# Kernel tuning notes

Hardware: AMD Instinct MI355X
Metric: run time of the kernel (lower is better)

The kernel has to match this reference:

```python
import jax, jax.numpy as jnp
import numpy as np

N_CLUSTERS = 512
TEMPERATURE = 0.1


def setup_inputs() -> dict:
    key = jax.random.key(0)
    k1, k2 = jax.random.split(key)
    x = jax.random.normal(k1, (32, 1024, 256), dtype=jnp.float32)
    centroids = jax.random.normal(k2, (N_CLUSTERS, 256), dtype=jnp.float32)
    return {"x": x, "centroids": centroids}


def reference(x, centroids):
    # Flatten non-cluster axes into a sample axis: [N, D]
    B, S, D = x.shape
    xf = x.reshape(-1, D)  # [N, D]
    x_sq = jnp.sum(xf * xf, axis=-1, keepdims=True)           # [N, 1]
    c_sq = jnp.sum(centroids * centroids, axis=-1)             # [K]
    cross = jnp.einsum('nd,kd->nk', xf, centroids)             # [N, K]
    dists = x_sq - 2.0 * cross + c_sq[None, :]                 # [N, K]
    # Temperature-scaled soft assignments
    assignments = jax.nn.softmax(-dists / TEMPERATURE, axis=-1)  # [N, K]
    # Restore leading (non-feature) dims, append cluster axis
    return assignments.reshape(B, S, N_CLUSTERS)
```

## Files before the change

kernel.cpp:

```cpp
#include <hip/hip_runtime.h>

#define NROWS 32768
#define KC 512
#define DDIM 256
#define BM 128
#define BK 32
#define KCH (DDIM / BK)
#define CHUNK_USH (KC * BK)

typedef __attribute__((ext_vector_type(8))) short bf16x8;
typedef __attribute__((ext_vector_type(4))) float f32x4;

union U8 { unsigned short u[8]; bf16x8 v; };

__device__ __forceinline__ unsigned short f2bf(float f) {
    union { float f; unsigned int u; } a; a.f = f;
    unsigned int r = a.u + 0x7fffu + ((a.u >> 16) & 1u);
    return (unsigned short)(r >> 16);
}
__device__ __forceinline__ float bf2f(unsigned short h) {
    union { unsigned int u; float f; } a; a.u = ((unsigned int)h) << 16;
    return a.f;
}
__device__ __forceinline__ void ld16(const void* g, void* l) {
    __builtin_amdgcn_global_load_lds(
        (const __attribute__((address_space(1))) unsigned int*)g,
        (__attribute__((address_space(3))) unsigned int*)l, 16, 0, 0);
}

__global__ __launch_bounds__(64) void prep_c(const float* __restrict__ c,
                                             unsigned short* __restrict__ bhi,
                                             unsigned short* __restrict__ blo,
                                             float* __restrict__ csq10) {
    const int n = blockIdx.x, lane = threadIdx.x;
    const int d0 = lane * 4;
    float4 v = ((const float4*)(c + (size_t)n * DDIM))[lane];
    float vv[4] = {v.x, v.y, v.z, v.w};
    unsigned short hh[4], ll[4];
    float ssq = 0.f;
    #pragma unroll
    for (int i = 0; i < 4; ++i) {
        ssq += vv[i] * vv[i];
        hh[i] = f2bf(vv[i]);
        ll[i] = f2bf(vv[i] - bf2f(hh[i]));
    }
    #pragma unroll
    for (int off = 32; off; off >>= 1) ssq += __shfl_xor(ssq, off);
    if (lane == 0) csq10[n] = 10.f * ssq;
    const int ks = d0 >> 5;
    const int q  = (d0 >> 3) & 3;
    const int s  = q ^ ((n >> 1) & 3);
    const size_t dst = (size_t)ks * CHUNK_USH + (n * 4 + s) * 8 + (d0 & 7);
    *(ushort4*)(bhi + dst) = make_ushort4(hh[0], hh[1], hh[2], hh[3]);
    *(ushort4*)(blo + dst) = make_ushort4(ll[0], ll[1], ll[2], ll[3]);
}

union SmemU {
    struct { unsigned short Bh[2][CHUNK_USH], Bl[2][CHUNK_USH]; } k;
    float lbuf[32 * 516];
};

__global__ __launch_bounds__(512, 2) void kmeans_mfma(
    const float* __restrict__ x, const unsigned short* __restrict__ bhi,
    const unsigned short* __restrict__ blo, const float* __restrict__ csq10,
    float* __restrict__ out) {
    __shared__ __align__(16) SmemU sm;
    __shared__ float red[2][2][BM];

    const int tid  = threadIdx.x;
    const int w    = tid >> 6, lane = tid & 63;
    const int wm   = w >> 1, wn = w & 1;
    const int cc   = lane & 15, q = lane >> 4;
    const int row0 = blockIdx.x * BM;

    f32x4 acc[2][16];
    #pragma unroll
    for (int mt = 0; mt < 2; ++mt)
        #pragma unroll
        for (int t = 0; t < 16; ++t) acc[mt][t] = (f32x4){0.f, 0.f, 0.f, 0.f};

    const float* xA0 = x + (size_t)(row0 + wm * 32 + cc) * DDIM + q * 8;
    const float* xA1 = xA0 + (size_t)16 * DDIM;
    const int sF = q ^ ((cc >> 1) & 3);
    const int bF = (4 * cc + sF) * 8;
    const int dmaOff = (w * 4) * 512;

    #pragma unroll
    for (int j = 0; j < 4; ++j) {
        const int o = dmaOff + j * 512;
        ld16(bhi + o + lane * 8, &sm.k.Bh[0][o]);
        ld16(blo + o + lane * 8, &sm.k.Bl[0][o]);
    }
    float4 c00 = *(const float4*)xA0;
    float4 c01 = *(const float4*)(xA0 + 4);
    float4 c10 = *(const float4*)xA1;
    float4 c11 = *(const float4*)(xA1 + 4);
    __syncthreads();

    for (int ks = 0; ks < KCH; ++ks) {
        const int pp = ks & 1;
        float4 n00, n01, n10, n11;
        if (ks < KCH - 1) {
            const size_t cb = (size_t)(ks + 1) * CHUNK_USH;
            #pragma unroll
            for (int j = 0; j < 4; ++j) {
                const int o = dmaOff + j * 512;
                ld16(bhi + cb + o + lane * 8, &sm.k.Bh[1 - pp][o]);
                ld16(blo + cb + o + lane * 8, &sm.k.Bl[1 - pp][o]);
            }
            const int kn = (ks + 1) * BK;
            n00 = *(const float4*)(xA0 + kn);
            n01 = *(const float4*)(xA0 + kn + 4);
            n10 = *(const float4*)(xA1 + kn);
            n11 = *(const float4*)(xA1 + kn + 4);
        }
        bf16x8 ah[2], al[2];
        {
            float v0[8] = {c00.x, c00.y, c00.z, c00.w, c01.x, c01.y, c01.z, c01.w};
            float v1[8] = {c10.x, c10.y, c10.z, c10.w, c11.x, c11.y, c11.z, c11.w};
            U8 H0, L0, H1, L1;
            #pragma unroll
            for (int i = 0; i < 8; ++i) {
                H0.u[i] = f2bf(v0[i]); L0.u[i] = f2bf(v0[i] - bf2f(H0.u[i]));
                H1.u[i] = f2bf(v1[i]); L1.u[i] = f2bf(v1[i] - bf2f(H1.u[i]));
            }
            ah[0] = H0.v; al[0] = L0.v; ah[1] = H1.v; al[1] = L1.v;
        }
        #pragma unroll
        for (int t = 0; t < 16; ++t) {
            const int bo = (wn * 16 + t) * 512 + bF;
            bf16x8 bh = *(const bf16x8*)&sm.k.Bh[pp][bo];
            bf16x8 bl = *(const bf16x8*)&sm.k.Bl[pp][bo];
            acc[0][t] = __builtin_amdgcn_mfma_f32_16x16x32_bf16(ah[0], bh, acc[0][t], 0, 0, 0);
            acc[1][t] = __builtin_amdgcn_mfma_f32_16x16x32_bf16(ah[1], bh, acc[1][t], 0, 0, 0);
            acc[0][t] = __builtin_amdgcn_mfma_f32_16x16x32_bf16(ah[0], bl, acc[0][t], 0, 0, 0);
            acc[1][t] = __builtin_amdgcn_mfma_f32_16x16x32_bf16(ah[1], bl, acc[1][t], 0, 0, 0);
            acc[0][t] = __builtin_amdgcn_mfma_f32_16x16x32_bf16(al[0], bh, acc[0][t], 0, 0, 0);
            acc[1][t] = __builtin_amdgcn_mfma_f32_16x16x32_bf16(al[1], bh, acc[1][t], 0, 0, 0);
        }
        c00 = n00; c01 = n01; c10 = n10; c11 = n11;
        __syncthreads();
    }

    float csqv[16];
    #pragma unroll
    for (int t = 0; t < 16; ++t) csqv[t] = csq10[wn * 256 + t * 16 + cc];
    const int rb = wm * 32 + q * 4;
    float M[2][4], I[2][4];
    #pragma unroll
    for (int mt = 0; mt < 2; ++mt)
        #pragma unroll
        for (int g = 0; g < 4; ++g) {
            float pm = -1e30f;
            #pragma unroll
            for (int t = 0; t < 16; ++t) pm = fmaxf(pm, 20.f * acc[mt][t][g] - csqv[t]);
            #pragma unroll
            for (int off = 1; off < 16; off <<= 1) pm = fmaxf(pm, __shfl_xor(pm, off));
            if (cc == 0) red[0][wn][rb + mt * 16 + g] = pm;
            M[mt][g] = pm;
        }
    __syncthreads();
    #pragma unroll
    for (int mt = 0; mt < 2; ++mt)
        #pragma unroll
        for (int g = 0; g < 4; ++g) {
            M[mt][g] = fmaxf(M[mt][g], red[0][1 - wn][rb + mt * 16 + g]);
            float ps = 0.f;
            #pragma unroll
            for (int t = 0; t < 16; ++t) ps += __expf(20.f * acc[mt][t][g] - csqv[t] - M[mt][g]);
            #pragma unroll
            for (int off = 1; off < 16; off <<= 1) ps += __shfl_xor(ps, off);
            if (cc == 0) red[1][wn][rb + mt * 16 + g] = ps;
        }
    __syncthreads();
    #pragma unroll
    for (int mt = 0; mt < 2; ++mt)
        #pragma unroll
        for (int g = 0; g < 4; ++g)
            I[mt][g] = 1.f / (red[1][0][rb + mt * 16 + g] + red[1][1][rb + mt * 16 + g]);

    #pragma unroll
    for (int p = 0; p < 4; ++p) {
        if (wm == p) {
            #pragma unroll
            for (int mt = 0; mt < 2; ++mt)
                #pragma unroll
                for (int g = 0; g < 4; ++g) {
                    const int   lr = mt * 16 + q * 4 + g;
                    const float mg = M[mt][g], ig = I[mt][g];
                    #pragma unroll
                    for (int t = 0; t < 16; ++t)
                        sm.lbuf[lr * 516 + wn * 256 + t * 16 + cc] =
                            __expf(20.f * acc[mt][t][g] - csqv[t] - mg) * ig;
                }
        }
        __syncthreads();
        #pragma unroll
        for (int j = 0; j < 8; ++j) {
            const int f    = j * 512 + tid;
            const int lrow = f >> 7;
            const int c4   = f & 127;
            float4    v    = *(const float4*)&sm.lbuf[lrow * 516 + c4 * 4];
            *(float4*)(out + (size_t)(row0 + p * 32 + lrow) * KC + c4 * 4) = v;
        }
        __syncthreads();
    }
}

extern "C" void kernel_launch(void* const* d_in, const int* in_sizes, int n_in,
                              void* d_out, int out_size, void* d_ws, size_t ws_size,
                              hipStream_t stream) {
    const float* x   = (const float*)d_in[0];
    const float* c   = (const float*)d_in[1];
    float*       out = (float*)d_out;

    unsigned short* bhi   = (unsigned short*)d_ws;
    unsigned short* blo   = bhi + (size_t)KCH * CHUNK_USH;
    float*          csq10 = (float*)(blo + (size_t)KCH * CHUNK_USH);

    prep_c<<<KC, 64, 0, stream>>>(c, bhi, blo, csq10);
    kmeans_mfma<<<NROWS / BM, 512, 0, stream>>>(x, bhi, blo, csq10, out);
}
```

Baseline: 118.6 us.

## Switch to 32x32x16 MFMA with smaller row tiles and 256-thread blocks

Replaces the 16x16x32 bf16 MFMA tiling with 32x32x16 MFMA instructions. Each wave now covers 32 rows by 256 clusters using 8 accumulator tiles. Block size drops to 64 rows and 256 threads, and the K chunk shrinks to 16, which halves the shared-memory B buffers and doubles the number of K iterations. The centroid prep layout and LDS swizzle are reworked to match the new operand layout, and the softmax reductions now precompute max and inverse sum into a shared table. The aim is to lower LDS traffic per FLOP and raise occupancy, at the cost of more barriers per row.

```diff
diff --git a/kernel.cpp b/kernel.cpp
--- a/kernel.cpp
+++ b/kernel.cpp
@@ -3,13 +3,13 @@
 #define NROWS 32768
 #define KC 512
 #define DDIM 256
-#define BM 128
-#define BK 32
+#define BM 64
+#define BK 16
 #define KCH (DDIM / BK)
 #define CHUNK_USH (KC * BK)
 
-typedef __attribute__((ext_vector_type(8))) short bf16x8;
-typedef __attribute__((ext_vector_type(4))) float f32x4;
+typedef __attribute__((ext_vector_type(8)))  short bf16x8;
+typedef __attribute__((ext_vector_type(16))) float f32x16;
 
 union U8 { unsigned short u[8]; bf16x8 v; };
 
@@ -47,42 +47,43 @@
     #pragma unroll
     for (int off = 32; off; off >>= 1) ssq += __shfl_xor(ssq, off);
     if (lane == 0) csq10[n] = 10.f * ssq;
-    const int ks = d0 >> 5;
-    const int q  = (d0 >> 3) & 3;
-    const int s  = q ^ ((n >> 1) & 3);
-    const size_t dst = (size_t)ks * CHUNK_USH + (n * 4 + s) * 8 + (d0 & 7);
+    const int ks = d0 >> 4;
+    const int h  = (d0 >> 3) & 1;
+    const int j0 = d0 & 7;
+    const int c5 = n & 31, tile = n >> 5;
+    const int p  = (2 * c5 + h) ^ ((c5 >> 2) & 1);
+    const size_t dst = (size_t)ks * CHUNK_USH + tile * 512 + p * 8 + j0;
     *(ushort4*)(bhi + dst) = make_ushort4(hh[0], hh[1], hh[2], hh[3]);
     *(ushort4*)(blo + dst) = make_ushort4(ll[0], ll[1], ll[2], ll[3]);
 }
 
 union SmemU {
     struct { unsigned short Bh[2][CHUNK_USH], Bl[2][CHUNK_USH]; } k;
-    float lbuf[32 * 516];
+    float lbuf[16 * 516];
 };
 
-__global__ __launch_bounds__(512, 2) void kmeans_mfma(
+__global__ __launch_bounds__(256, 2) void kmeans_mfma(
     const float* __restrict__ x, const unsigned short* __restrict__ bhi,
     const unsigned short* __restrict__ blo, const float* __restrict__ csq10,
     float* __restrict__ out) {
     __shared__ __align__(16) SmemU sm;
-    __shared__ float red[2][2][BM];
+    __shared__ float  red0[2][BM], red1[2][BM];
+    __shared__ float2 MI[BM];
 
     const int tid  = threadIdx.x;
     const int w    = tid >> 6, lane = tid & 63;
     const int wm   = w >> 1, wn = w & 1;
-    const int cc   = lane & 15, q = lane >> 4;
+    const int c5   = lane & 31, h = lane >> 5;
     const int row0 = blockIdx.x * BM;
 
-    f32x4 acc[2][16];
-    #pragma unroll
-    for (int mt = 0; mt < 2; ++mt)
-        #pragma unroll
-        for (int t = 0; t < 16; ++t) acc[mt][t] = (f32x4){0.f, 0.f, 0.f, 0.f};
-
-    const float* xA0 = x + (size_t)(row0 + wm * 32 + cc) * DDIM + q * 8;
-    const float* xA1 = xA0 + (size_t)16 * DDIM;
-    const int sF = q ^ ((cc >> 1) & 3);
-    const int bF = (4 * cc + sF) * 8;
+    f32x16 acc[8];
+    #pragma unroll
+    for (int t = 0; t < 8; ++t)
+        #pragma unroll
+        for (int r = 0; r < 16; ++r) acc[t][r] = 0.f;
+
+    const float* xrow = x + (size_t)(row0 + wm * 32 + c5) * DDIM + h * 8;
+    const int bRd    = ((2 * c5 + h) ^ ((c5 >> 2) & 1)) * 8;
     const int dmaOff = (w * 4) * 512;
 
     #pragma unroll
@@ -91,15 +92,13 @@
         ld16(bhi + o + lane * 8, &sm.k.Bh[0][o]);
         ld16(blo + o + lane * 8, &sm.k.Bl[0][o]);
     }
-    float4 c00 = *(const float4*)xA0;
-    float4 c01 = *(const float4*)(xA0 + 4);
-    float4 c10 = *(const float4*)xA1;
-    float4 c11 = *(const float4*)(xA1 + 4);
+    float4 a0 = *(const float4*)xrow;
+    float4 a1 = *(const float4*)(xrow + 4);
     __syncthreads();
 
     for (int ks = 0; ks < KCH; ++ks) {
         const int pp = ks & 1;
-        float4 n00, n01, n10, n11;
+        float4 n0, n1;
         if (ks < KCH - 1) {
             const size_t cb = (size_t)(ks + 1) * CHUNK_USH;
             #pragma unroll
@@ -108,100 +107,88 @@
                 ld16(bhi + cb + o + lane * 8, &sm.k.Bh[1 - pp][o]);
                 ld16(blo + cb + o + lane * 8, &sm.k.Bl[1 - pp][o]);
             }
-            const int kn = (ks + 1) * BK;
-            n00 = *(const float4*)(xA0 + kn);
-            n01 = *(const float4*)(xA0 + kn + 4);
-            n10 = *(const float4*)(xA1 + kn);
-            n11 = *(const float4*)(xA1 + kn + 4);
-        }
-        bf16x8 ah[2], al[2];
+            n0 = *(const float4*)(xrow + (ks + 1) * BK);
+            n1 = *(const float4*)(xrow + (ks + 1) * BK + 4);
+        }
+        bf16x8 ah, al;
         {
-            float v0[8] = {c00.x, c00.y, c00.z, c00.w, c01.x, c01.y, c01.z, c01.w};
-            float v1[8] = {c10.x, c10.y, c10.z, c10.w, c11.x, c11.y, c11.z, c11.w};
-            U8 H0, L0, H1, L1;
+            float v8[8] = {a0.x, a0.y, a0.z, a0.w, a1.x, a1.y, a1.z, a1.w};
+            U8 H, L;
             #pragma unroll
             for (int i = 0; i < 8; ++i) {
-                H0.u[i] = f2bf(v0[i]); L0.u[i] = f2bf(v0[i] - bf2f(H0.u[i]));
-                H1.u[i] = f2bf(v1[i]); L1.u[i] = f2bf(v1[i] - bf2f(H1.u[i]));
+                H.u[i] = f2bf(v8[i]);
+                L.u[i] = f2bf(v8[i] - bf2f(H.u[i]));
             }
-            ah[0] = H0.v; al[0] = L0.v; ah[1] = H1.v; al[1] = L1.v;
-        }
-        #pragma unroll
-        for (int t = 0; t < 16; ++t) {
-            const int bo = (wn * 16 + t) * 512 + bF;
+            ah = H.v; al = L.v;
+        }
+        #pragma unroll
+        for (int t = 0; t < 8; ++t) {
+            const int bo = (wn * 8 + t) * 512 + bRd;
             bf16x8 bh = *(const bf16x8*)&sm.k.Bh[pp][bo];
             bf16x8 bl = *(const bf16x8*)&sm.k.Bl[pp][bo];
-            acc[0][t] = __builtin_amdgcn_mfma_f32_16x16x32_bf16(ah[0], bh, acc[0][t], 0, 0, 0);
-            acc[1][t] = __builtin_amdgcn_mfma_f32_16x16x32_bf16(ah[1], bh, acc[1][t], 0, 0, 0);
-            acc[0][t] = __builtin_amdgcn_mfma_f32_16x16x32_bf16(ah[0], bl, acc[0][t], 0, 0, 0);
-            acc[1][t] = __builtin_amdgcn_mfma_f32_16x16x32_bf16(ah[1], bl, acc[1][t], 0, 0, 0);
-            acc[0][t] = __builtin_amdgcn_mfma_f32_16x16x32_bf16(al[0], bh, acc[0][t], 0, 0, 0);
-            acc[1][t] = __builtin_amdgcn_mfma_f32_16x16x32_bf16(al[1], bh, acc[1][t], 0, 0, 0);
-        }
-        c00 = n00; c01 = n01; c10 = n10; c11 = n11;
+            acc[t] = __builtin_amdgcn_mfma_f32_32x32x16_bf16(ah, bh, acc[t], 0, 0, 0);
+            acc[t] = __builtin_amdgcn_mfma_f32_32x32x16_bf16(ah, bl, acc[t], 0, 0, 0);
+            acc[t] = __builtin_amdgcn_mfma_f32_32x32x16_bf16(al, bh, acc[t], 0, 0, 0);
+        }
+        a0 = n0; a1 = n1;
         __syncthreads();
     }
 
-    float csqv[16];
-    #pragma unroll
-    for (int t = 0; t < 16; ++t) csqv[t] = csq10[wn * 256 + t * 16 + cc];
-    const int rb = wm * 32 + q * 4;
-    float M[2][4], I[2][4];
-    #pragma unroll
-    for (int mt = 0; mt < 2; ++mt)
-        #pragma unroll
-        for (int g = 0; g < 4; ++g) {
-            float pm = -1e30f;
+    float csqv[8];
+    #pragma unroll
+    for (int t = 0; t < 8; ++t) csqv[t] = csq10[wn * 256 + t * 32 + c5];
+
+    #pragma unroll
+    for (int r = 0; r < 16; ++r) {
+        float pm = -1e30f;
+        #pragma unroll
+        for (int t = 0; t < 8; ++t) pm = fmaxf(pm, 20.f * acc[t][r] - csqv[t]);
+        #pragma unroll
+        for (int off = 1; off < 32; off <<= 1) pm = fmaxf(pm, __shfl_xor(pm, off));
+        if (c5 == 0) red0[wn][wm * 32 + (r & 3) + 8 * (r >> 2) + 4 * h] = pm;
+    }
+    __syncthreads();
+    #pragma unroll
+    for (int r = 0; r < 16; ++r) {
+        const int row = wm * 32 + (r & 3) + 8 * (r >> 2) + 4 * h;
+        const float Mf = fmaxf(red0[0][row], red0[1][row]);
+        float ps = 0.f;
+        #pragma unroll
+        for (int t = 0; t < 8; ++t) ps += __expf(20.f * acc[t][r] - csqv[t] - Mf);
+        #pragma unroll
+        for (int off = 1; off < 32; off <<= 1) ps += __shfl_xor(ps, off);
+        if (c5 == 0) red1[wn][row] = ps;
+    }
+    __syncthreads();
+    if (tid < BM) {
+        const float Mf = fmaxf(red0[0][tid], red0[1][tid]);
+        const float Sf = red1[0][tid] + red1[1][tid];
+        MI[tid] = make_float2(Mf, 1.f / Sf);
+    }
+    __syncthreads();
+
+    #pragma unroll
+    for (int p = 0; p < 4; ++p) {
+        if (wm == (p >> 1)) {
             #pragma unroll
-            for (int t = 0; t < 16; ++t) pm = fmaxf(pm, 20.f * acc[mt][t][g] - csqv[t]);
-            #pragma unroll
-            for (int off = 1; off < 16; off <<= 1) pm = fmaxf(pm, __shfl_xor(pm, off));
-            if (cc == 0) red[0][wn][rb + mt * 16 + g] = pm;
-            M[mt][g] = pm;
-        }
-    __syncthreads();
-    #pragma unroll
-    for (int mt = 0; mt < 2; ++mt)
-        #pragma unroll
-        for (int g = 0; g < 4; ++g) {
-            M[mt][g] = fmaxf(M[mt][g], red[0][1 - wn][rb + mt * 16 + g]);
-            float ps = 0.f;
-            #pragma unroll
-            for (int t = 0; t < 16; ++t) ps += __expf(20.f * acc[mt][t][g] - csqv[t] - M[mt][g]);
-            #pragma unroll
-            for (int off = 1; off < 16; off <<= 1) ps += __shfl_xor(ps, off);
-            if (cc == 0) red[1][wn][rb + mt * 16 + g] = ps;
-        }
-    __syncthreads();
-    #pragma unroll
-    for (int mt = 0; mt < 2; ++mt)
-        #pragma unroll
-        for (int g = 0; g < 4; ++g)
-            I[mt][g] = 1.f / (red[1][0][rb + mt * 16 + g] + red[1][1][rb + mt * 16 + g]);
-
-    #pragma unroll
-    for (int p = 0; p < 4; ++p) {
-        if (wm == p) {
-            #pragma unroll
-            for (int mt = 0; mt < 2; ++mt)
+            for (int i = 0; i < 8; ++i) {
+                const int    rr  = (p & 1) * 8 + i;
+                const int    lr  = (i & 3) + 8 * (i >> 2) + 4 * h;
+                const float2 mi  = MI[p * 16 + lr];
                 #pragma unroll
-                for (int g = 0; g < 4; ++g) {
-                    const int   lr = mt * 16 + q * 4 + g;
-                    const float mg = M[mt][g], ig = I[mt][g];
-                    #pragma unroll
-                    for (int t = 0; t < 16; ++t)
-                        sm.lbuf[lr * 516 + wn * 256 + t * 16 + cc] =
-                            __expf(20.f * acc[mt][t][g] - csqv[t] - mg) * ig;
-                }
+                for (int t = 0; t < 8; ++t)
+                    sm.lbuf[lr * 516 + wn * 256 + t * 32 + c5] =
+                        __expf(20.f * acc[t][rr] - csqv[t] - mi.x) * mi.y;
+            }
         }
         __syncthreads();
         #pragma unroll
         for (int j = 0; j < 8; ++j) {
-            const int f    = j * 512 + tid;
+            const int f    = j * 256 + tid;
             const int lrow = f >> 7;
             const int c4   = f & 127;
             float4    v    = *(const float4*)&sm.lbuf[lrow * 516 + c4 * 4];
-            *(float4*)(out + (size_t)(row0 + p * 32 + lrow) * KC + c4 * 4) = v;
+            *(float4*)(out + (size_t)(row0 + p * 16 + lrow) * KC + c4 * 4) = v;
         }
         __syncthreads();
     }
@@ -219,5 +206,5 @@
     float*          csq10 = (float*)(blo + (size_t)KCH * CHUNK_USH);
 
     prep_c<<<KC, 64, 0, stream>>>(c, bhi, blo, csq10);
-    kmeans_mfma<<<NROWS / BM, 512, 0, stream>>>(x, bhi, blo, csq10, out);
-}
+    kmeans_mfma<<<NROWS / BM, 256, 0, stream>>>(x, bhi, blo, csq10, out);
+}
```

After: 123.0 us. 1.04x slower.

## Reshape warp tiling to 2x4 with 64-row by 128-cluster tiles per warp

Applied to the files above, without the earlier changes.

Changes the warp layout from 4x2 (32 rows by 256 clusters per warp) to 2x4 (64 rows by 128 clusters per warp). Each warp now converts four A fragments and reads eight B fragments from LDS per k-chunk instead of two and sixteen. This cuts LDS B traffic per MFMA and raises reuse of each B load across four M tiles. It also makes the softmax reduction four-way across warps, adding an MI shared array and an extra barrier, and raises register pressure for the A fragments.

```diff
diff --git a/kernel.cpp b/kernel.cpp
--- a/kernel.cpp
+++ b/kernel.cpp
@@ -65,22 +65,25 @@
     const unsigned short* __restrict__ blo, const float* __restrict__ csq10,
     float* __restrict__ out) {
     __shared__ __align__(16) SmemU sm;
-    __shared__ float red[2][2][BM];
+    __shared__ float  red0[4][BM], red1[4][BM];
+    __shared__ float2 MI[BM];
 
     const int tid  = threadIdx.x;
     const int w    = tid >> 6, lane = tid & 63;
-    const int wm   = w >> 1, wn = w & 1;
+    const int wm   = w >> 2, wn = w & 3;
     const int cc   = lane & 15, q = lane >> 4;
     const int row0 = blockIdx.x * BM;
 
-    f32x4 acc[2][16];
-    #pragma unroll
-    for (int mt = 0; mt < 2; ++mt)
-        #pragma unroll
-        for (int t = 0; t < 16; ++t) acc[mt][t] = (f32x4){0.f, 0.f, 0.f, 0.f};
-
-    const float* xA0 = x + (size_t)(row0 + wm * 32 + cc) * DDIM + q * 8;
-    const float* xA1 = xA0 + (size_t)16 * DDIM;
+    f32x4 acc[4][8];
+    #pragma unroll
+    for (int mt = 0; mt < 4; ++mt)
+        #pragma unroll
+        for (int t = 0; t < 8; ++t) acc[mt][t] = (f32x4){0.f, 0.f, 0.f, 0.f};
+
+    const float* xA[4];
+    #pragma unroll
+    for (int mt = 0; mt < 4; ++mt)
+        xA[mt] = x + (size_t)(row0 + wm * 64 + mt * 16 + cc) * DDIM + q * 8;
     const int sF = q ^ ((cc >> 1) & 3);
     const int bF = (4 * cc + sF) * 8;
     const int dmaOff = (w * 4) * 512;
@@ -91,15 +94,17 @@
         ld16(bhi + o + lane * 8, &sm.k.Bh[0][o]);
         ld16(blo + o + lane * 8, &sm.k.Bl[0][o]);
     }
-    float4 c00 = *(const float4*)xA0;
-    float4 c01 = *(const float4*)(xA0 + 4);
-    float4 c10 = *(const float4*)xA1;
-    float4 c11 = *(const float4*)(xA1 + 4);
+    float4 a[4][2];
+    #pragma unroll
+    for (int mt = 0; mt < 4; ++mt) {
+        a[mt][0] = *(const float4*)(xA[mt]);
+        a[mt][1] = *(const float4*)(xA[mt] + 4);
+    }
     __syncthreads();
 
     for (int ks = 0; ks < KCH; ++ks) {
         const int pp = ks & 1;
-        float4 n00, n01, n10, n11;
+        float4 n[4][2];
         if (ks < KCH - 1) {
             const size_t cb = (size_t)(ks + 1) * CHUNK_USH;
             #pragma unroll
@@ -109,90 +114,99 @@
                 ld16(blo + cb + o + lane * 8, &sm.k.Bl[1 - pp][o]);
             }
             const int kn = (ks + 1) * BK;
-            n00 = *(const float4*)(xA0 + kn);
-            n01 = *(const float4*)(xA0 + kn + 4);
-            n10 = *(const float4*)(xA1 + kn);
-            n11 = *(const float4*)(xA1 + kn + 4);
-        }
-        bf16x8 ah[2], al[2];
-        {
-            float v0[8] = {c00.x, c00.y, c00.z, c00.w, c01.x, c01.y, c01.z, c01.w};
-            float v1[8] = {c10.x, c10.y, c10.z, c10.w, c11.x, c11.y, c11.z, c11.w};
-            U8 H0, L0, H1, L1;
+            #pragma unroll
+            for (int mt = 0; mt < 4; ++mt) {
+                n[mt][0] = *(const float4*)(xA[mt] + kn);
+                n[mt][1] = *(const float4*)(xA[mt] + kn + 4);
+            }
+        }
+        bf16x8 ah[4], al[4];
+        #pragma unroll
+        for (int mt = 0; mt < 4; ++mt) {
+            float v8[8] = {a[mt][0].x, a[mt][0].y, a[mt][0].z, a[mt][0].w,
+                           a[mt][1].x, a[mt][1].y, a[mt][1].z, a[mt][1].w};
+            U8 H, L;
             #pragma unroll
             for (int i = 0; i < 8; ++i) {
-                H0.u[i] = f2bf(v0[i]); L0.u[i] = f2bf(v0[i] - bf2f(H0.u[i]));
-                H1.u[i] = f2bf(v1[i]); L1.u[i] = f2bf(v1[i] - bf2f(H1.u[i]));
-            }
-            ah[0] = H0.v; al[0] = L0.v; ah[1] = H1.v; al[1] = L1.v;
-        }
-        #pragma unroll
-        for (int t = 0; t < 16; ++t) {
-            const int bo = (wn * 16 + t) * 512 + bF;
+                H.u[i] = f2bf(v8[i]);
+                L.u[i] = f2bf(v8[i] - bf2f(H.u[i]));
+            }
+            ah[mt] = H.v; al[mt] = L.v;
+        }
+        #pragma unroll
+        for (int t = 0; t < 8; ++t) {
+            const int bo = (wn * 8 + t) * 512 + bF;
             bf16x8 bh = *(const bf16x8*)&sm.k.Bh[pp][bo];
             bf16x8 bl = *(const bf16x8*)&sm.k.Bl[pp][bo];
-            acc[0][t] = __builtin_amdgcn_mfma_f32_16x16x32_bf16(ah[0], bh, acc[0][t], 0, 0, 0);
-            acc[1][t] = __builtin_amdgcn_mfma_f32_16x16x32_bf16(ah[1], bh, acc[1][t], 0, 0, 0);
-            acc[0][t] = __builtin_amdgcn_mfma_f32_16x16x32_bf16(ah[0], bl, acc[0][t], 0, 0, 0);
-            acc[1][t] = __builtin_amdgcn_mfma_f32_16x16x32_bf16(ah[1], bl, acc[1][t], 0, 0, 0);
-            acc[0][t] = __builtin_amdgcn_mfma_f32_16x16x32_bf16(al[0], bh, acc[0][t], 0, 0, 0);
-            acc[1][t] = __builtin_amdgcn_mfma_f32_16x16x32_bf16(al[1], bh, acc[1][t], 0, 0, 0);
-        }
-        c00 = n00; c01 = n01; c10 = n10; c11 = n11;
+            #pragma unroll
+            for (int mt = 0; mt < 4; ++mt) {
+                acc[mt][t] = __builtin_amdgcn_mfma_f32_16x16x32_bf16(ah[mt], bh, acc[mt][t], 0, 0, 0);
+                acc[mt][t] = __builtin_amdgcn_mfma_f32_16x16x32_bf16(ah[mt], bl, acc[mt][t], 0, 0, 0);
+                acc[mt][t] = __builtin_amdgcn_mfma_f32_16x16x32_bf16(al[mt], bh, acc[mt][t], 0, 0, 0);
+            }
+        }
+        #pragma unroll
+        for (int mt = 0; mt < 4; ++mt) { a[mt][0] = n[mt][0]; a[mt][1] = n[mt][1]; }
         __syncthreads();
     }
 
-    float csqv[16];
-    #pragma unroll
-    for (int t = 0; t < 16; ++t) csqv[t] = csq10[wn * 256 + t * 16 + cc];
-    const int rb = wm * 32 + q * 4;
-    float M[2][4], I[2][4];
-    #pragma unroll
-    for (int mt = 0; mt < 2; ++mt)
+    float csqv[8];
+    #pragma unroll
+    for (int t = 0; t < 8; ++t) csqv[t] = csq10[wn * 128 + t * 16 + cc];
+
+    #pragma unroll
+    for (int mt = 0; mt < 4; ++mt)
         #pragma unroll
         for (int g = 0; g < 4; ++g) {
             float pm = -1e30f;
             #pragma unroll
-            for (int t = 0; t < 16; ++t) pm = fmaxf(pm, 20.f * acc[mt][t][g] - csqv[t]);
+            for (int t = 0; t < 8; ++t) pm = fmaxf(pm, 20.f * acc[mt][t][g] - csqv[t]);
             #pragma unroll
             for (int off = 1; off < 16; off <<= 1) pm = fmaxf(pm, __shfl_xor(pm, off));
-            if (cc == 0) red[0][wn][rb + mt * 16 + g] = pm;
-            M[mt][g] = pm;
-        }
-    __syncthreads();
-    #pragma unroll
-    for (int mt = 0; mt < 2; ++mt)
+            if (cc == 0) red0[wn][wm * 64 + mt * 16 + q * 4 + g] = pm;
+        }
+    __syncthreads();
+    float M[4][4];
+    #pragma unroll
+    for (int mt = 0; mt < 4; ++mt)
         #pragma unroll
         for (int g = 0; g < 4; ++g) {
-            M[mt][g] = fmaxf(M[mt][g], red[0][1 - wn][rb + mt * 16 + g]);
+            const int row = wm * 64 + mt * 16 + q * 4 + g;
+            float Mf = fmaxf(fmaxf(red0[0][row], red0[1][row]),
+                             fmaxf(red0[2][row], red0[3][row]));
+            M[mt][g] = Mf;
             float ps = 0.f;
             #pragma unroll
-            for (int t = 0; t < 16; ++t) ps += __expf(20.f * acc[mt][t][g] - csqv[t] - M[mt][g]);
+            for (int t = 0; t < 8; ++t) ps += __expf(20.f * acc[mt][t][g] - csqv[t] - Mf);
             #pragma unroll
             for (int off = 1; off < 16; off <<= 1) ps += __shfl_xor(ps, off);
-            if (cc == 0) red[1][wn][rb + mt * 16 + g] = ps;
-        }
-    __syncthreads();
-    #pragma unroll
-    for (int mt = 0; mt < 2; ++mt)
-        #pragma unroll
-        for (int g = 0; g < 4; ++g)
-            I[mt][g] = 1.f / (red[1][0][rb + mt * 16 + g] + red[1][1][rb + mt * 16 + g]);
+            if (cc == 0) red1[wn][row] = ps;
+        }
+    __syncthreads();
+    if (tid < BM) {
+        const float Mf = fmaxf(fmaxf(red0[0][tid], red0[1][tid]),
+                               fmaxf(red0[2][tid], red0[3][tid]));
+        const float Sf = red1[0][tid] + red1[1][tid] + red1[2][tid] + red1[3][tid];
+        MI[tid] = make_float2(Mf, 1.f / Sf);
+    }
+    __syncthreads();
 
     #pragma unroll
     for (int p = 0; p < 4; ++p) {
-        if (wm == p) {
-            #pragma unroll
-            for (int mt = 0; mt < 2; ++mt)
+        if (wm == (p >> 1)) {
+            #pragma unroll
+            for (int mi = 0; mi < 2; ++mi) {
+                const int mt = (p & 1) * 2 + mi;
                 #pragma unroll
                 for (int g = 0; g < 4; ++g) {
-                    const int   lr = mt * 16 + q * 4 + g;
-                    const float mg = M[mt][g], ig = I[mt][g];
+                    const int    lr  = mi * 16 + q * 4 + g;
+                    const float2 mi2 = MI[p * 32 + lr];
                     #pragma unroll
-                    for (int t = 0; t < 16; ++t)
-                        sm.lbuf[lr * 516 + wn * 256 + t * 16 + cc] =
-                            __expf(20.f * acc[mt][t][g] - csqv[t] - mg) * ig;
+                    for (int t = 0; t < 8; ++t)
+                        sm.lbuf[lr * 516 + wn * 128 + t * 16 + cc] =
+                            __expf(20.f * acc[mt][t][g] - csqv[t] - mi2.x) * mi2.y;
                 }
+            }
         }
         __syncthreads();
         #pragma unroll
```

Result: slower. 129.0 us (+8.8%).
